# Kernel optimization log

Measured on AMD Instinct MI355X. Metric: run time of the kernel, lower is better.

The kernel has to match this reference:

```python
import jax, jax.numpy as jnp
import numpy as np

N, E, IN, HID, OUT, L = 50000, 800000, 128, 64, 40, 3


def setup_inputs() -> dict:
    key = jax.random.key(0)
    ks = jax.random.split(key, 10)
    x = jax.random.normal(ks[0], (N, IN), jnp.float32)
    edge_index = jax.random.randint(ks[1], (2, E), 0, N, dtype=jnp.int32)

    def u(k, shape, fan_in):
        s = 1.0 / np.sqrt(fan_in)
        return jax.random.uniform(k, shape, jnp.float32, -s, s)

    return {
        "x": x,
        "edge_index": edge_index,
        # former1 (NWGformerF): in -> hidden projection
        "Wf": u(ks[2], (IN, HID), IN),
        "bf": jnp.zeros((HID,), jnp.float32),
        # stacked GCNConv weights (hidden->hidden)
        "conv_W": u(ks[3], (L, HID, HID), HID),
        "conv_b": jnp.zeros((L, HID), jnp.float32),
        # residual linears
        "lin_W": u(ks[4], (L, HID, HID), HID),
        "lin_b": u(ks[5], (L, HID), HID),
        # batchnorm (eval mode: affine with running stats)
        "gamma": jnp.ones((L, HID), jnp.float32),
        "beta": jnp.zeros((L, HID), jnp.float32),
        "run_mean": jnp.zeros((L, HID), jnp.float32),
        "run_var": jnp.ones((L, HID), jnp.float32),
        # output head
        "pred_W": u(ks[6], (HID, OUT), HID),
        "pred_b": jnp.zeros((OUT,), jnp.float32),
    }


def reference(x, edge_index, Wf, bf, conv_W, conv_b, lin_W, lin_b,
              gamma, beta, run_mean, run_var, pred_W, pred_b):
    n = x.shape[0]
    src, dst = edge_index[0], edge_index[1]
    eps = 1e-5

    # GCN symmetric normalization with self-loops: deg over dst (+1 self loop)
    deg = jax.ops.segment_sum(jnp.ones(src.shape[0], x.dtype), dst,
                              num_segments=n) + 1.0
    dinv = jax.lax.rsqrt(deg)                      # [N]
    edge_coef = dinv[src] * dinv[dst]              # [E]
    self_coef = (dinv * dinv)[:, None]             # [N,1]

    def gcn(h, W, b):
        hw = h @ W                                 # [N,HID]
        agg = jax.ops.segment_sum(hw[src] * edge_coef[:, None], dst,
                                  num_segments=n)
        return agg + hw * self_coef + b

    # former1: in -> hidden (dropout is identity in eval mode)
    h = x @ Wf + bf

    for i in range(L):
        h = gcn(h, conv_W[i], conv_b[i]) + h @ lin_W[i] + lin_b[i]  # res
        h = (h - run_mean[i]) * (gamma[i] * jax.lax.rsqrt(run_var[i] + eps)) + beta[i]
        h = jax.nn.relu(h)

    return h @ pred_W + pred_b
```

## Files before the change

kernel.cpp:

```cpp
#include <hip/hip_runtime.h>
#include <hip/hip_bf16.h>
#include <hip/hip_fp16.h>

#define IN_DIM 128
#define HID 64
#define OUT_DIM 40
#define SPAD 68
#define NB_HIST 256

typedef __hip_bfloat16 bf16;
typedef unsigned short u16;
typedef _Float16 f16;
typedef __attribute__((ext_vector_type(8))) _Float16 f16x8;
typedef __attribute__((ext_vector_type(4))) float f32x4;

__device__ __forceinline__ float b2f(bf16 v) { return __bfloat162float(v); }
__device__ __forceinline__ float relu_f(float x) { return 0.5f * (x + fabsf(x)); }
__device__ __forceinline__ float ldv(const void* p, int i, int is32) {
    return is32 ? ((const float*)p)[i] : b2f(((const bf16*)p)[i]);
}

__global__ void MPNNs_60198261620971_kernel() {}

__global__ void canary_k(float* out, int m) {
    int i = blockIdx.x * blockDim.x + threadIdx.x;
    if (i < m) out[i] = 1234.0f;
}

__global__ void detect_k(const unsigned int* __restrict__ rv, int* __restrict__ flag) {
    if (threadIdx.x == 0 && blockIdx.x == 0)
        flag[0] = (rv[0] == 0x3F800000u) ? 1 : 0;
}


__global__ __launch_bounds__(256) void histform_k(const int* __restrict__ dst,
                                                  unsigned int* __restrict__ cnt,
                                                  u16* __restrict__ rank,
                                                  int e, int n, int n2, int chunk, int npass,
                                                  const void* __restrict__ x,
                                                  const void* __restrict__ Wf,
                                                  const void* __restrict__ bfv,
                                                  const int* __restrict__ dflag,
                                                  float* __restrict__ h) {
    __shared__ __align__(16) unsigned int shmem[16384];
    if (blockIdx.x < NB_HIST) {
        int b = blockIdx.x;
        int e0 = b * chunk, e1 = min(e, e0 + chunk);
        for (int p = 0; p < npass; p++) {
            int w0 = p << 14, w1 = min(n2, w0 + 16384);
            for (int i = threadIdx.x; i < 16384; i += 256) shmem[i] = 0;
            __syncthreads();
            for (int i = e0 + threadIdx.x; i < e1; i += 256) {
                int d = dst[i];
                if ((unsigned)d < (unsigned)n) {
                    int w = d >> 1;
                    if (w >= w0 && w < w1) {
                        int sh = (d & 1) * 16;
                        unsigned old = atomicAdd(&shmem[w - w0], 1u << sh);
                        rank[i] = (u16)((old >> sh) & 0xFFFFu);
                    }
                } else if (p == 0) {
                    rank[i] = 0;
                }
            }
            __syncthreads();
            for (int i = threadIdx.x; i < (w1 - w0); i += 256)
                cnt[(size_t)b * n2 + w0 + i] = shmem[i];
            __syncthreads();
        }
        return;
    }
    f16 (*wT)[IN_DIM + 8] = (f16(*)[IN_DIM + 8])shmem;
    int is32 = dflag[0];
    for (int i = threadIdx.x; i < IN_DIM * HID; i += 256) {
        int k = i >> 6, nn = i & 63;
        wT[nn][k] = (f16)ldv(Wf, i, is32);
    }
    __syncthreads();
    int wave = threadIdx.x >> 6, lane = threadIdx.x & 63;
    int m = lane & 15, quad = lane >> 4;
    int row0 = (int)(blockIdx.x - NB_HIST) * 64 + wave * 16;
    if (row0 >= n) return;
    int ar = row0 + m;
    int arc = (ar < n) ? ar : (n - 1);
    f16x8 a[4];
    if (is32) {
        const float* xp = (const float*)x + (size_t)arc * IN_DIM;
        #pragma unroll
        for (int cn = 0; cn < 4; cn++) {
            float4 u0 = *(const float4*)(xp + cn * 32 + quad * 8);
            float4 u1 = *(const float4*)(xp + cn * 32 + quad * 8 + 4);
            a[cn] = (f16x8){ (f16)u0.x, (f16)u0.y, (f16)u0.z, (f16)u0.w,
                             (f16)u1.x, (f16)u1.y, (f16)u1.z, (f16)u1.w };
        }
    } else {
        const bf16* xp = (const bf16*)x + (size_t)arc * IN_DIM;
        #pragma unroll
        for (int cn = 0; cn < 4; cn++)
            #pragma unroll
            for (int j = 0; j < 8; j++) a[cn][j] = (f16)b2f(xp[cn * 32 + quad * 8 + j]);
    }
    f32x4 acc[4];
    #pragma unroll
    for (int ct = 0; ct < 4; ct++) acc[ct] = (f32x4){0.f, 0.f, 0.f, 0.f};
    #pragma unroll
    for (int ct = 0; ct < 4; ct++) {
        int nn = ct * 16 + m;
        #pragma unroll
        for (int cn = 0; cn < 4; cn++) {
            f16x8 b = *(const f16x8*)&wT[nn][cn * 32 + quad * 8];
            acc[ct] = __builtin_amdgcn_mfma_f32_16x16x32_f16(a[cn], b, acc[ct], 0, 0, 0);
        }
    }
    float bias[4];
    #pragma unroll
    for (int ct = 0; ct < 4; ct++) bias[ct] = ldv(bfv, ct * 16 + m, is32);
    #pragma unroll
    for (int r = 0; r < 4; r++) {
        int row = row0 + quad * 4 + r;
        if (row < n) {
            #pragma unroll
            for (int ct = 0; ct < 4; ct++)
                h[(size_t)row * HID + ct * 16 + m] = acc[ct][r] + bias[ct];
        }
    }
}

__global__ void scanB_k(unsigned int* __restrict__ cnt, unsigned int* __restrict__ c2,
                        int n2) {
    int t = blockIdx.x * blockDim.x + threadIdx.x;
    if (t >= n2) return;
    unsigned acc0 = 0, acc1 = 0;
    size_t idx = t;
    for (int b = 0; b < NB_HIST; b += 8) {
        unsigned w[8];
        #pragma unroll
        for (int j = 0; j < 8; j++) w[j] = cnt[idx + (size_t)j * n2];
        #pragma unroll
        for (int j = 0; j < 8; j++) {
            cnt[idx + (size_t)j * n2] = acc0 | (acc1 << 16);
            acc0 += w[j] & 0xFFFFu;
            acc1 += w[j] >> 16;
        }
        idx += (size_t)8 * n2;
    }
    c2[t] = acc0 | (acc1 << 16);
}

__global__ void scan1_k(const unsigned int* __restrict__ c2, int* __restrict__ row_ptr,
                        int* __restrict__ psum, float* __restrict__ dinv, int n) {
    __shared__ int sdata[1024];
    int i = blockIdx.x * 1024 + threadIdx.x;
    int v = 0;
    if (i < n) {
        v = (int)((c2[i >> 1] >> ((i & 1) * 16)) & 0xFFFFu);
        dinv[i] = rsqrtf((float)v + 1.0f);
    }
    sdata[threadIdx.x] = v;
    __syncthreads();
    for (int off = 1; off < 1024; off <<= 1) {
        int t = (threadIdx.x >= off) ? sdata[threadIdx.x - off] : 0;
        __syncthreads();
        sdata[threadIdx.x] += t;
        __syncthreads();
    }
    if (i < n) row_ptr[i] = sdata[threadIdx.x] - v;
    if (threadIdx.x == 1023) psum[blockIdx.x] = sdata[1023];
}

__global__ void scan2_k(int* __restrict__ psum, int* __restrict__ row_ptr, int nb, int n) {
    __shared__ int sdata[1024];
    int v = (threadIdx.x < nb) ? psum[threadIdx.x] : 0;
    sdata[threadIdx.x] = v;
    __syncthreads();
    for (int off = 1; off < 1024; off <<= 1) {
        int t = (threadIdx.x >= off) ? sdata[threadIdx.x - off] : 0;
        __syncthreads();
        sdata[threadIdx.x] += t;
        __syncthreads();
    }
    if (threadIdx.x < nb) psum[threadIdx.x] = sdata[threadIdx.x] - v;
    if (threadIdx.x == 1023) row_ptr[n] = sdata[1023];
}

__global__ void scan3_k(int* __restrict__ row_ptr, const int* __restrict__ psum, int n) {
    int i = blockIdx.x * blockDim.x + threadIdx.x;
    if (i < n) row_ptr[i] += psum[i >> 10];
}

__global__ __launch_bounds__(256) void filldense_k(const int* __restrict__ src,
                                                   const int* __restrict__ dst,
                                                   const int* __restrict__ row_ptr,
                                                   const unsigned int* __restrict__ cnt,
                                                   const u16* __restrict__ rank,
                                                   u16* __restrict__ col,
                                                   int e, int n, int n2, int chunk,
                                                   float* __restrict__ h,
                                                   const void* __restrict__ convW,
                                                   const void* __restrict__ linW,
                                                   const void* __restrict__ convB,
                                                   const void* __restrict__ linB,
                                                   const int* __restrict__ dflag,
                                                   const float* __restrict__ dinv,
                                                   __half* __restrict__ hws) {
    __shared__ __align__(16) f16 wT2[2][HID][72];
    if (blockIdx.x < NB_HIST) {
        int b = blockIdx.x;
        int e0 = b * chunk, e1 = min(e, e0 + chunk);
        for (int i = e0 + threadIdx.x; i < e1; i += 256) {
            int d = dst[i];
            if ((unsigned)d < (unsigned)n) {
                unsigned bw = cnt[(size_t)b * n2 + (d >> 1)];
                int base = (int)((bw >> ((d & 1) * 16)) & 0xFFFFu);
                col[row_ptr[d] + base + (int)rank[i]] = (u16)src[i];
            }
        }
        return;
    }
    int is32 = dflag[0];
    for (int i = threadIdx.x; i < HID * HID; i += 256) {
        int k = i >> 6, nn = i & 63;
        wT2[0][nn][k] = (f16)ldv(convW, i, is32);
        wT2[1][nn][k] = (f16)ldv(linW, i, is32);
    }
    __syncthreads();
    int wave = threadIdx.x >> 6, lane = threadIdx.x & 63;
    int m = lane & 15, quad = lane >> 4;
    int row0 = (int)(blockIdx.x - NB_HIST) * 64 + wave * 16;
    if (row0 >= n) return;
    int ar = row0 + m;
    const float* hp = h + (size_t)((ar < n) ? ar : 0) * HID;
    float4 v0 = *(const float4*)(hp + quad * 8);
    float4 v1 = *(const float4*)(hp + quad * 8 + 4);
    float4 v2 = *(const float4*)(hp + 32 + quad * 8);
    float4 v3 = *(const float4*)(hp + 32 + quad * 8 + 4);
    f16x8 a0 = { (f16)v0.x, (f16)v0.y, (f16)v0.z, (f16)v0.w,
                 (f16)v1.x, (f16)v1.y, (f16)v1.z, (f16)v1.w };
    f16x8 a1 = { (f16)v2.x, (f16)v2.y, (f16)v2.z, (f16)v2.w,
                 (f16)v3.x, (f16)v3.y, (f16)v3.z, (f16)v3.w };
    f32x4 acc[2][4];
    #pragma unroll
    for (int t = 0; t < 2; t++)
        #pragma unroll
        for (int ct = 0; ct < 4; ct++) acc[t][ct] = (f32x4){0.f, 0.f, 0.f, 0.f};
    #pragma unroll
    for (int ct = 0; ct < 4; ct++) {
        int nn = ct * 16 + m;
        f16x8 b00 = *(const f16x8*)&wT2[0][nn][quad * 8];
        f16x8 b01 = *(const f16x8*)&wT2[0][nn][32 + quad * 8];
        f16x8 b10 = *(const f16x8*)&wT2[1][nn][quad * 8];
        f16x8 b11 = *(const f16x8*)&wT2[1][nn][32 + quad * 8];
        acc[0][ct] = __builtin_amdgcn_mfma_f32_16x16x32_f16(a0, b00, acc[0][ct], 0, 0, 0);
        acc[0][ct] = __builtin_amdgcn_mfma_f32_16x16x32_f16(a1, b01, acc[0][ct], 0, 0, 0);
        acc[1][ct] = __builtin_amdgcn_mfma_f32_16x16x32_f16(a0, b10, acc[1][ct], 0, 0, 0);
        acc[1][ct] = __builtin_amdgcn_mfma_f32_16x16x32_f16(a1, b11, acc[1][ct], 0, 0, 0);
    }
    float cbv[4];
    #pragma unroll
    for (int ct = 0; ct < 4; ct++)
        cbv[ct] = ldv(convB, ct * 16 + m, is32) + ldv(linB, ct * 16 + m, is32);
    #pragma unroll
    for (int r = 0; r < 4; r++) {
        int row = row0 + quad * 4 + r;
        if (row < n) {
            float dv = dinv[row];
            #pragma unroll
            for (int ct = 0; ct < 4; ct++) {
                int colx = ct * 16 + m;
                hws[(size_t)row * HID + colx] = __float2half(acc[0][ct][r] * dv);
                h[(size_t)row * HID + colx] = acc[1][ct][r] + cbv[ct];
            }
        }
    }
}

__global__ __launch_bounds__(256) void dense_k(float* __restrict__ h,
                                               const void* __restrict__ convW,
                                               const void* __restrict__ linW,
                                               const void* __restrict__ convB,
                                               const void* __restrict__ linB,
                                               const int* __restrict__ dflag,
                                               const float* __restrict__ dinv,
                                               __half* __restrict__ hws, int n, int l) {
    __shared__ __align__(16) f16 wT2[2][HID][72];
    int is32 = dflag[0];
    int wOff = l * HID * HID, vOff = l * HID;
    for (int i = threadIdx.x; i < HID * HID; i += 256) {
        int k = i >> 6, nn = i & 63;
        wT2[0][nn][k] = (f16)ldv(convW, wOff + i, is32);
        wT2[1][nn][k] = (f16)ldv(linW, wOff + i, is32);
    }
    __syncthreads();
    int wave = threadIdx.x >> 6, lane = threadIdx.x & 63;
    int m = lane & 15, quad = lane >> 4;
    int row0 = blockIdx.x * 64 + wave * 16;
    if (row0 >= n) return;
    int ar = row0 + m;
    const float* hp = h + (size_t)((ar < n) ? ar : 0) * HID;
    float4 v0 = *(const float4*)(hp + quad * 8);
    float4 v1 = *(const float4*)(hp + quad * 8 + 4);
    float4 v2 = *(const float4*)(hp + 32 + quad * 8);
    float4 v3 = *(const float4*)(hp + 32 + quad * 8 + 4);
    f16x8 a0 = { (f16)v0.x, (f16)v0.y, (f16)v0.z, (f16)v0.w,
                 (f16)v1.x, (f16)v1.y, (f16)v1.z, (f16)v1.w };
    f16x8 a1 = { (f16)v2.x, (f16)v2.y, (f16)v2.z, (f16)v2.w,
                 (f16)v3.x, (f16)v3.y, (f16)v3.z, (f16)v3.w };
    f32x4 acc[2][4];
    #pragma unroll
    for (int t = 0; t < 2; t++)
        #pragma unroll
        for (int ct = 0; ct < 4; ct++) acc[t][ct] = (f32x4){0.f, 0.f, 0.f, 0.f};
    #pragma unroll
    for (int ct = 0; ct < 4; ct++) {
        int nn = ct * 16 + m;
        f16x8 b00 = *(const f16x8*)&wT2[0][nn][quad * 8];
        f16x8 b01 = *(const f16x8*)&wT2[0][nn][32 + quad * 8];
        f16x8 b10 = *(const f16x8*)&wT2[1][nn][quad * 8];
        f16x8 b11 = *(const f16x8*)&wT2[1][nn][32 + quad * 8];
        acc[0][ct] = __builtin_amdgcn_mfma_f32_16x16x32_f16(a0, b00, acc[0][ct], 0, 0, 0);
        acc[0][ct] = __builtin_amdgcn_mfma_f32_16x16x32_f16(a1, b01, acc[0][ct], 0, 0, 0);
        acc[1][ct] = __builtin_amdgcn_mfma_f32_16x16x32_f16(a0, b10, acc[1][ct], 0, 0, 0);
        acc[1][ct] = __builtin_amdgcn_mfma_f32_16x16x32_f16(a1, b11, acc[1][ct], 0, 0, 0);
    }
    float cbv[4];
    #pragma unroll
    for (int ct = 0; ct < 4; ct++)
        cbv[ct] = ldv(convB, vOff + ct * 16 + m, is32) + ldv(linB, vOff + ct * 16 + m, is32);
    #pragma unroll
    for (int r = 0; r < 4; r++) {
        int row = row0 + quad * 4 + r;
        if (row < n) {
            float dv = dinv[row];
            #pragma unroll
            for (int ct = 0; ct < 4; ct++) {
                int colx = ct * 16 + m;
                hws[(size_t)row * HID + colx] = __float2half(acc[0][ct][r] * dv);
                h[(size_t)row * HID + colx] = acc[1][ct][r] + cbv[ct];
            }
        }
    }
}

__global__ __launch_bounds__(256) void agg_k(const __half* __restrict__ hws,
                                             const float* __restrict__ dinv,
                                             const int* __restrict__ row_ptr,
                                             const u16* __restrict__ col,
                                             const void* __restrict__ gamma,
                                             const void* __restrict__ beta,
                                             const void* __restrict__ mean,
                                             const void* __restrict__ var,
                                             const int* __restrict__ dflag,
                                             float* __restrict__ h, int n, int l) {
    int gwave = (blockIdx.x * blockDim.x + threadIdx.x) >> 6;
    int lane = threadIdx.x & 63;
    int nw = (gridDim.x * blockDim.x) >> 6;
    int half = lane >> 5, c = lane & 31;
    const __half2* hws2 = (const __half2*)hws;
    int is32 = dflag[0];
    int vOff = l * HID;
    float mn0 = ldv(mean, vOff + 2 * c, is32),     mn1 = ldv(mean, vOff + 2 * c + 1, is32);
    float sc0 = ldv(gamma, vOff + 2 * c, is32) * rsqrtf(ldv(var, vOff + 2 * c, is32) + 1e-5f);
    float sc1 = ldv(gamma, vOff + 2 * c + 1, is32) * rsqrtf(ldv(var, vOff + 2 * c + 1, is32) + 1e-5f);
    float bt0 = ldv(beta, vOff + 2 * c, is32),     bt1 = ldv(beta, vOff + 2 * c + 1, is32);
    for (int v = gwave; v < n; v += nw) {
        int s0 = row_ptr[v], s1 = row_ptr[v + 1];
        float2 a[8];
        #pragma unroll
        for (int g = 0; g < 8; g++) a[g] = make_float2(0.f, 0.f);
        if (half == 0) {
            float2 s = __half22float2(hws2[(size_t)v * 32 + c]);
            a[0].x += s.x; a[0].y += s.y;
        }
        for (int j0 = s0; j0 < s1; j0 += 64) {
            int myidx = (j0 + lane < s1) ? (int)col[j0 + lane] : 0;
            int cnt = min(64, s1 - j0);
            int t = 0;
            for (; t + 16 <= cnt; t += 16) {
                #pragma unroll
                for (int g = 0; g < 8; g++) {
                    int idx = __shfl(myidx, t + 2 * g + half);
                    idx = ((unsigned)idx < (unsigned)n) ? idx : 0;
                    float2 p = __half22float2(hws2[(size_t)idx * 32 + c]);
                    a[g].x += p.x; a[g].y += p.y;
                }
            }
            for (; t < cnt; t += 2) {
                int has = (t + half) < cnt;
                int sel = t + half; if (sel >= cnt) sel = cnt - 1;
                int idx = __shfl(myidx, sel);
                idx = ((unsigned)idx < (unsigned)n) ? idx : 0;
                float2 p = __half22float2(hws2[(size_t)idx * 32 + c]);
                if (has) { a[0].x += p.x; a[0].y += p.y; }
            }
        }
        float ax = ((a[0].x + a[1].x) + (a[2].x + a[3].x)) + ((a[4].x + a[5].x) + (a[6].x + a[7].x));
        float ay = ((a[0].y + a[1].y) + (a[2].y + a[3].y)) + ((a[4].y + a[5].y) + (a[6].y + a[7].y));
        float px = __shfl(ax, c + 32);
        float py = __shfl(ay, c + 32);
        if (half == 0) {
            float dv = dinv[v];
            float2 basev = *(const float2*)&h[(size_t)v * HID + 2 * c];
            float vx = dv * (ax + px) + basev.x;
            float vy = dv * (ay + py) + basev.y;
            vx = (vx - mn0) * sc0 + bt0;
            vy = (vy - mn1) * sc1 + bt1;
            float2 o = make_float2(relu_f(vx), relu_f(vy));
            *(float2*)&h[(size_t)v * HID + 2 * c] = o;
        }
    }
}

__global__ __launch_bounds__(256) void pred_k(const float* __restrict__ h,
                                              const void* __restrict__ pW,
                                              const void* __restrict__ pb,
                                              const int* __restrict__ dflag,
                                              void* __restrict__ out, int n) {
    __shared__ float sW[HID * OUT_DIM];
    __shared__ float sh[64 * SPAD];
    int is32 = dflag[0];
    if (is32) {
        const float4* w4 = (const float4*)pW;
        for (int i = threadIdx.x; i < HID * OUT_DIM / 4; i += 256) ((float4*)sW)[i] = w4[i];
    } else {
        for (int i = threadIdx.x; i < HID * OUT_DIM; i += 256) sW[i] = b2f(((const bf16*)pW)[i]);
    }
    int tid = threadIdx.x, cg = tid & 15, rg = tid >> 4;
    int rowBase = blockIdx.x * 64;
    #pragma unroll
    for (int pass = 0; pass < 4; pass++) {
        int r = pass * 16 + (tid >> 4);
        int c = (tid & 15) * 4;
        int gr = rowBase + r;
        float4 v = (gr < n) ? *(const float4*)&h[(size_t)gr * HID + c] : make_float4(0.f, 0.f, 0.f, 0.f);
        *(float4*)&sh[r * SPAD + c] = v;
    }
    __syncthreads();
    if (cg < 10) {
        float acc[4][4];
        #pragma unroll
        for (int i = 0; i < 4; i++)
            #pragma unroll
            for (int j = 0; j < 4; j++) acc[i][j] = 0.f;
        for (int k = 0; k < 64; k += 4) {
            float4 hr[4], w[4];
            #pragma unroll
            for (int i = 0; i < 4; i++) hr[i] = *(float4*)&sh[(rg * 4 + i) * SPAD + k];
            #pragma unroll
            for (int j = 0; j < 4; j++) w[j] = *(float4*)&sW[(k + j) * OUT_DIM + cg * 4];
            #pragma unroll
            for (int i = 0; i < 4; i++) {
                const float* hh = (const float*)&hr[i];
                #pragma unroll
                for (int j = 0; j < 4; j++) {
                    const float* ww = (const float*)&w[j];
                    acc[i][0] += hh[j] * ww[0];
                    acc[i][1] += hh[j] * ww[1];
                    acc[i][2] += hh[j] * ww[2];
                    acc[i][3] += hh[j] * ww[3];
                }
            }
        }
        float b0 = ldv(pb, cg * 4 + 0, is32), b1 = ldv(pb, cg * 4 + 1, is32);
        float b2 = ldv(pb, cg * 4 + 2, is32), b3 = ldv(pb, cg * 4 + 3, is32);
        #pragma unroll
        for (int i = 0; i < 4; i++) {
            int r = rowBase + rg * 4 + i;
            if (r < n) {
                if (is32) {
                    float4 o = make_float4(acc[i][0] + b0, acc[i][1] + b1, acc[i][2] + b2, acc[i][3] + b3);
                    *(float4*)((float*)out + (size_t)r * OUT_DIM + cg * 4) = o;
                } else {
                    bf16* ob = (bf16*)out + (size_t)r * OUT_DIM + cg * 4;
                    ob[0] = __float2bfloat16(acc[i][0] + b0);
                    ob[1] = __float2bfloat16(acc[i][1] + b1);
                    ob[2] = __float2bfloat16(acc[i][2] + b2);
                    ob[3] = __float2bfloat16(acc[i][3] + b3);
                }
            }
        }
    }
}


extern "C" void kernel_launch(void* const* d_in, const int* in_sizes, int n_in,
                              void* d_out, int out_size, void* d_ws, size_t ws_size,
                              hipStream_t stream) {
    const void* x     = d_in[0];
    const int*  ei    = (const int*)d_in[1];
    const void* Wf    = d_in[2];
    const void* bfv   = d_in[3];
    const void* convW = d_in[4];
    const void* convB = d_in[5];
    const void* linW  = d_in[6];
    const void* linB  = d_in[7];
    const void* gamma = d_in[8];
    const void* beta  = d_in[9];
    const void* rmean = d_in[10];
    const void* rvar  = d_in[11];
    const void* pW    = d_in[12];
    const void* pb    = d_in[13];

    const int n = in_sizes[0] / IN_DIM;
    const int e = in_sizes[1] / 2;
    const int L = in_sizes[5] / HID;
    const int n2 = (n + 1) / 2;

    const int* src = ei;
    const int* dst = ei + e;

    char* ws = (char*)d_ws;
    size_t off = 0;
    auto take = [&](size_t bytes) {
        char* p = ws + off;
        off = (off + bytes + 255) & ~(size_t)255;
        return p;
    };
    float*        h       = (float*)take((size_t)n * HID * 4);
    __half*       hws     = (__half*)take((size_t)n * HID * 2);
    float*        dinv    = (float*)take((size_t)n * 4);
    unsigned int* c2      = (unsigned int*)take((size_t)n2 * 4);
    unsigned int* cnt     = (unsigned int*)take((size_t)NB_HIST * n2 * 4);
    int*          row_ptr = (int*)take((size_t)(n + 1) * 4);
    u16*          rank    = (u16*)take((size_t)e * 2);
    u16*          colbuf  = (u16*)take((size_t)e * 2);
    int*          psum    = (int*)take(1024 * 4);
    int*          dflag   = (int*)take(256);

    if (off > ws_size || n > 65535) {
        canary_k<<<(out_size + 255) / 256, 256, 0, stream>>>((float*)d_out, out_size);
        return;
    }

    const int nblocks = (n + 255) / 256;
    const int nb1024  = (n + 1023) / 1024;
    const int nb64    = (n + 63) / 64;
    const int chunk   = (((e + NB_HIST - 1) / NB_HIST) + 255) & ~255;
    const int npass   = (n2 + 16383) / 16384;

    detect_k<<<1, 64, 0, stream>>>((const unsigned int*)rvar, dflag);
    histform_k<<<NB_HIST + nb64, 256, 0, stream>>>(dst, cnt, rank, e, n, n2, chunk, npass,
                                                   x, Wf, bfv, dflag, h);
    scanB_k<<<(n2 + 255) / 256, 256, 0, stream>>>(cnt, c2, n2);
    scan1_k<<<nb1024, 1024, 0, stream>>>(c2, row_ptr, psum, dinv, n);
    scan2_k<<<1, 1024, 0, stream>>>(psum, row_ptr, nb1024, n);
    scan3_k<<<nblocks, 256, 0, stream>>>(row_ptr, psum, n);
    filldense_k<<<NB_HIST + nb64, 256, 0, stream>>>(src, dst, row_ptr, cnt, rank, colbuf,
                                                    e, n, n2, chunk, h, convW, linW,
                                                    convB, linB, dflag, dinv, hws);
    for (int l = 0; l < L; l++) {
        if (l > 0)
            dense_k<<<nb64, 256, 0, stream>>>(h, convW, linW, convB, linB,
                                              dflag, dinv, hws, n, l);
        agg_k<<<2048, 256, 0, stream>>>(hws, dinv, row_ptr, colbuf,
                                        gamma, beta, rmean, rvar, dflag, h, n, l);
    }

    pred_k<<<nb64, 256, 0, stream>>>(h, pW, pb, dflag, (void*)d_out, n);
}
```

Before: 314.9 us.

## Restructure CSR build: split histogram by node halves, merge column scan into scan1

The histogram kernel now uses 128 edge chunks, each split across two blocks that cover different halves of the node range, instead of 256 chunk blocks each making multiple passes. The dtype detection is folded into the histogram kernel, and the input projection moves to its own kernel. The per-node column scan over chunks is merged into the first row-pointer scan, which removes a separate kernel and the c2 buffer. The aim is fewer launches and less cnt traffic, at the cost of each block reading its whole edge chunk twice and the hist and projection work no longer sharing one launch. The two-half split only covers n2 up to 32768, so it relies on n being at most 65535; adding the 16-bit halves as a single unsigned word assumes neither half overflows.

After: 306.8 us (median of 2 runs). 2.6% less time.

```diff
diff --git a/kernel.cpp b/kernel.cpp
--- a/kernel.cpp
+++ b/kernel.cpp
@@ -6,7 +6,7 @@
 #define HID 64
 #define OUT_DIM 40
 #define SPAD 68
-#define NB_HIST 256
+#define CHUNKS 128
 
 typedef __hip_bfloat16 bf16;
 typedef unsigned short u16;
@@ -27,50 +27,46 @@
     if (i < m) out[i] = 1234.0f;
 }
 
-__global__ void detect_k(const unsigned int* __restrict__ rv, int* __restrict__ flag) {
-    if (threadIdx.x == 0 && blockIdx.x == 0)
+
+__global__ __launch_bounds__(256) void hist_k(const int* __restrict__ dst,
+                                              unsigned int* __restrict__ cnt,
+                                              u16* __restrict__ rank,
+                                              int e, int n, int n2, int chunk,
+                                              const unsigned int* __restrict__ rv,
+                                              int* __restrict__ flag) {
+    __shared__ unsigned int hc[16384];
+    if (blockIdx.x == 0 && threadIdx.x == 0)
         flag[0] = (rv[0] == 0x3F800000u) ? 1 : 0;
-}
-
-
-__global__ __launch_bounds__(256) void histform_k(const int* __restrict__ dst,
-                                                  unsigned int* __restrict__ cnt,
-                                                  u16* __restrict__ rank,
-                                                  int e, int n, int n2, int chunk, int npass,
-                                                  const void* __restrict__ x,
-                                                  const void* __restrict__ Wf,
-                                                  const void* __restrict__ bfv,
-                                                  const int* __restrict__ dflag,
-                                                  float* __restrict__ h) {
-    __shared__ __align__(16) unsigned int shmem[16384];
-    if (blockIdx.x < NB_HIST) {
-        int b = blockIdx.x;
-        int e0 = b * chunk, e1 = min(e, e0 + chunk);
-        for (int p = 0; p < npass; p++) {
-            int w0 = p << 14, w1 = min(n2, w0 + 16384);
-            for (int i = threadIdx.x; i < 16384; i += 256) shmem[i] = 0;
-            __syncthreads();
-            for (int i = e0 + threadIdx.x; i < e1; i += 256) {
-                int d = dst[i];
-                if ((unsigned)d < (unsigned)n) {
-                    int w = d >> 1;
-                    if (w >= w0 && w < w1) {
-                        int sh = (d & 1) * 16;
-                        unsigned old = atomicAdd(&shmem[w - w0], 1u << sh);
-                        rank[i] = (u16)((old >> sh) & 0xFFFFu);
-                    }
-                } else if (p == 0) {
-                    rank[i] = 0;
-                }
-            }
-            __syncthreads();
-            for (int i = threadIdx.x; i < (w1 - w0); i += 256)
-                cnt[(size_t)b * n2 + w0 + i] = shmem[i];
-            __syncthreads();
-        }
-        return;
-    }
-    f16 (*wT)[IN_DIM + 8] = (f16(*)[IN_DIM + 8])shmem;
+    int c = blockIdx.x >> 1, hf = blockIdx.x & 1;
+    int w0 = hf << 14;
+    int w1 = min(n2, w0 + 16384);
+    int nw = w1 - w0;
+    if (nw <= 0) return;
+    for (int i = threadIdx.x; i < nw; i += 256) hc[i] = 0;
+    __syncthreads();
+    int e0 = c * chunk, e1 = min(e, e0 + chunk);
+    for (int i = e0 + threadIdx.x; i < e1; i += 256) {
+        int d = dst[i];
+        if ((unsigned)d < (unsigned)n) {
+            int w = d >> 1;
+            if (w >= w0 && w < w1) {
+                int sh = (d & 1) * 16;
+                unsigned old = atomicAdd(&hc[w - w0], 1u << sh);
+                rank[i] = (u16)((old >> sh) & 0xFFFFu);
+            }
+        }
+    }
+    __syncthreads();
+    for (int i = threadIdx.x; i < nw; i += 256)
+        cnt[(size_t)c * n2 + w0 + i] = hc[i];
+}
+
+__global__ __launch_bounds__(256) void former_k(const void* __restrict__ x,
+                                                const void* __restrict__ Wf,
+                                                const void* __restrict__ bfv,
+                                                const int* __restrict__ dflag,
+                                                float* __restrict__ h, int n) {
+    __shared__ __align__(16) f16 wT[HID][IN_DIM + 8];
     int is32 = dflag[0];
     for (int i = threadIdx.x; i < IN_DIM * HID; i += 256) {
         int k = i >> 6, nn = i & 63;
@@ -79,7 +75,7 @@
     __syncthreads();
     int wave = threadIdx.x >> 6, lane = threadIdx.x & 63;
     int m = lane & 15, quad = lane >> 4;
-    int row0 = (int)(blockIdx.x - NB_HIST) * 64 + wave * 16;
+    int row0 = blockIdx.x * 64 + wave * 16;
     if (row0 >= n) return;
     int ar = row0 + m;
     int arc = (ar < n) ? ar : (n - 1);
@@ -126,46 +122,47 @@
     }
 }
 
-__global__ void scanB_k(unsigned int* __restrict__ cnt, unsigned int* __restrict__ c2,
-                        int n2) {
-    int t = blockIdx.x * blockDim.x + threadIdx.x;
-    if (t >= n2) return;
-    unsigned acc0 = 0, acc1 = 0;
-    size_t idx = t;
-    for (int b = 0; b < NB_HIST; b += 8) {
-        unsigned w[8];
-        #pragma unroll
-        for (int j = 0; j < 8; j++) w[j] = cnt[idx + (size_t)j * n2];
-        #pragma unroll
-        for (int j = 0; j < 8; j++) {
-            cnt[idx + (size_t)j * n2] = acc0 | (acc1 << 16);
-            acc0 += w[j] & 0xFFFFu;
-            acc1 += w[j] >> 16;
-        }
-        idx += (size_t)8 * n2;
-    }
-    c2[t] = acc0 | (acc1 << 16);
-}
-
-__global__ void scan1_k(const unsigned int* __restrict__ c2, int* __restrict__ row_ptr,
-                        int* __restrict__ psum, float* __restrict__ dinv, int n) {
+__global__ void scan1B_k(unsigned int* __restrict__ cnt, int* __restrict__ row_ptr,
+                         int* __restrict__ psum, float* __restrict__ dinv,
+                         int n, int n2) {
+    __shared__ unsigned int tot[512];
     __shared__ int sdata[1024];
-    int i = blockIdx.x * 1024 + threadIdx.x;
+    int tid = threadIdx.x;
+    int w = blockIdx.x * 512 + tid;
+    if (tid < 512) {
+        unsigned acc = 0;
+        if (w < n2) {
+            size_t idx = w;
+            for (int b = 0; b < CHUNKS; b += 8) {
+                unsigned ww[8];
+                #pragma unroll
+                for (int j = 0; j < 8; j++) ww[j] = cnt[idx + (size_t)(b + j) * n2];
+                #pragma unroll
+                for (int j = 0; j < 8; j++) {
+                    cnt[idx + (size_t)(b + j) * n2] = acc;
+                    acc += ww[j];
+                }
+            }
+        }
+        tot[tid] = acc;
+    }
+    __syncthreads();
+    int i = blockIdx.x * 1024 + tid;
     int v = 0;
     if (i < n) {
-        v = (int)((c2[i >> 1] >> ((i & 1) * 16)) & 0xFFFFu);
+        v = (int)((tot[tid >> 1] >> ((tid & 1) * 16)) & 0xFFFFu);
         dinv[i] = rsqrtf((float)v + 1.0f);
     }
-    sdata[threadIdx.x] = v;
+    sdata[tid] = v;
     __syncthreads();
     for (int off = 1; off < 1024; off <<= 1) {
-        int t = (threadIdx.x >= off) ? sdata[threadIdx.x - off] : 0;
+        int t = (tid >= off) ? sdata[tid - off] : 0;
         __syncthreads();
-        sdata[threadIdx.x] += t;
+        sdata[tid] += t;
         __syncthreads();
     }
-    if (i < n) row_ptr[i] = sdata[threadIdx.x] - v;
-    if (threadIdx.x == 1023) psum[blockIdx.x] = sdata[1023];
+    if (i < n) row_ptr[i] = sdata[tid] - v;
+    if (tid == 1023) psum[blockIdx.x] = sdata[1023];
 }
 
 __global__ void scan2_k(int* __restrict__ psum, int* __restrict__ row_ptr, int nb, int n) {
@@ -204,7 +201,7 @@
                                                    const float* __restrict__ dinv,
                                                    __half* __restrict__ hws) {
     __shared__ __align__(16) f16 wT2[2][HID][72];
-    if (blockIdx.x < NB_HIST) {
+    if (blockIdx.x < CHUNKS) {
         int b = blockIdx.x;
         int e0 = b * chunk, e1 = min(e, e0 + chunk);
         for (int i = e0 + threadIdx.x; i < e1; i += 256) {
@@ -226,7 +223,7 @@
     __syncthreads();
     int wave = threadIdx.x >> 6, lane = threadIdx.x & 63;
     int m = lane & 15, quad = lane >> 4;
-    int row0 = (int)(blockIdx.x - NB_HIST) * 64 + wave * 16;
+    int row0 = (int)(blockIdx.x - CHUNKS) * 64 + wave * 16;
     if (row0 >= n) return;
     int ar = row0 + m;
     const float* hp = h + (size_t)((ar < n) ? ar : 0) * HID;
@@ -518,8 +515,7 @@
     float*        h       = (float*)take((size_t)n * HID * 4);
     __half*       hws     = (__half*)take((size_t)n * HID * 2);
     float*        dinv    = (float*)take((size_t)n * 4);
-    unsigned int* c2      = (unsigned int*)take((size_t)n2 * 4);
-    unsigned int* cnt     = (unsigned int*)take((size_t)NB_HIST * n2 * 4);
+    unsigned int* cnt     = (unsigned int*)take((size_t)CHUNKS * n2 * 4);
     int*          row_ptr = (int*)take((size_t)(n + 1) * 4);
     u16*          rank    = (u16*)take((size_t)e * 2);
     u16*          colbuf  = (u16*)take((size_t)e * 2);
@@ -534,19 +530,17 @@
     const int nblocks = (n + 255) / 256;
     const int nb1024  = (n + 1023) / 1024;
     const int nb64    = (n + 63) / 64;
-    const int chunk   = (((e + NB_HIST - 1) / NB_HIST) + 255) & ~255;
-    const int npass   = (n2 + 16383) / 16384;
-
-    detect_k<<<1, 64, 0, stream>>>((const unsigned int*)rvar, dflag);
-    histform_k<<<NB_HIST + nb64, 256, 0, stream>>>(dst, cnt, rank, e, n, n2, chunk, npass,
-                                                   x, Wf, bfv, dflag, h);
-    scanB_k<<<(n2 + 255) / 256, 256, 0, stream>>>(cnt, c2, n2);
-    scan1_k<<<nb1024, 1024, 0, stream>>>(c2, row_ptr, psum, dinv, n);
+    const int chunk   = (((e + CHUNKS - 1) / CHUNKS) + 255) & ~255;
+
+    hist_k<<<2 * CHUNKS, 256, 0, stream>>>(dst, cnt, rank, e, n, n2, chunk,
+                                           (const unsigned int*)rvar, dflag);
+    former_k<<<nb64, 256, 0, stream>>>(x, Wf, bfv, dflag, h, n);
+    scan1B_k<<<nb1024, 1024, 0, stream>>>(cnt, row_ptr, psum, dinv, n, n2);
     scan2_k<<<1, 1024, 0, stream>>>(psum, row_ptr, nb1024, n);
     scan3_k<<<nblocks, 256, 0, stream>>>(row_ptr, psum, n);
-    filldense_k<<<NB_HIST + nb64, 256, 0, stream>>>(src, dst, row_ptr, cnt, rank, colbuf,
-                                                    e, n, n2, chunk, h, convW, linW,
-                                                    convB, linB, dflag, dinv, hws);
+    filldense_k<<<CHUNKS + nb64, 256, 0, stream>>>(src, dst, row_ptr, cnt, rank, colbuf,
+                                                   e, n, n2, chunk, h, convW, linW,
+                                                   convB, linB, dflag, dinv, hws);
     for (int l = 0; l < L; l++) {
         if (l > 0)
             dense_k<<<nb64, 256, 0, stream>>>(h, convW, linW, convB, linB,
```
